# Kernel optimization log

Measured on AMD Instinct MI355X. Metric: run time of the kernel, lower is better.

Reference implementation:

```python
import jax, jax.numpy as jnp
import numpy as np

D = 100  # hidden dim: kernel has 3*D = 300 entries (concat(a, b, a*b))


def setup_inputs() -> dict:
    key = jax.random.key(0)
    k1, k2, k3 = jax.random.split(key, 3)
    context = jax.random.normal(k1, (16384, D), dtype=jnp.float32)
    question = jax.random.normal(k2, (4096, D), dtype=jnp.float32)
    kernel = jax.random.normal(k3, (3 * D,), dtype=jnp.float32)
    return {"context": context, "question": question, "kernel": kernel}


def reference(context, question, kernel):
    # kernel . concat(a, b, a*b) = a.w1 + b.w2 + (a*b).w3, computed without
    # materializing the [N, M, 3D] feature tensor.
    w1, w2, w3 = kernel[:D], kernel[D:2 * D], kernel[2 * D:]
    # S: [N, M] similarity matrix
    S = (context @ w1)[:, None] + (question @ w2)[None, :] \
        + (context * w3) @ question.T
    # C2Q: row-softmax over question positions, weighted sum of question
    A = jax.nn.softmax(S, axis=-1)            # [N, M]
    U_A = A @ question                          # [N, D]
    # Q2C: softmax over per-row maxes, weighted sum of context, tiled to rows
    b = jax.nn.softmax(jnp.max(S, axis=-1))    # [N]
    h = b @ context                             # [D]
    H_A = jnp.broadcast_to(h, context.shape)   # [N, D]
    # megamerge: [N, 4D]
    G = jnp.concatenate([context, U_A, context * U_A, context * H_A], axis=-1)
    return G
```

## Files before the change

### kernel.cpp

```cpp
#include <hip/hip_runtime.h>

typedef _Float16 f16x8 __attribute__((ext_vector_type(8)));
typedef float    f32x4 __attribute__((ext_vector_type(4)));
typedef float    f32x16 __attribute__((ext_vector_type(16)));
typedef unsigned int u32;

#define N_CTX 16384
#define N_Q   4096
#define DIM   100
#define THR   4.0f

union FragU { unsigned int u[4]; f16x8 v; };

#define MFMA32(a, b, c) __builtin_amdgcn_mfma_f32_32x32x16_f16((a), (b), (c), 0, 0, 0)
#define GLOAD_LDS(g, l) __builtin_amdgcn_global_load_lds( \
    (const __attribute__((address_space(1))) u32*)(const void*)(g), \
    (__attribute__((address_space(3))) u32*)(void*)(l), 16, 0, 0)

__global__ void prep_all(const float* __restrict__ q, const float* __restrict__ ctx,
                         const float* __restrict__ ker,
                         unsigned short* __restrict__ qbS, unsigned short* __restrict__ qTS,
                         unsigned short* __restrict__ cbH, float* __restrict__ a) {
    int b = blockIdx.x;
    int tid = threadIdx.x;
    if (b < 16) {
        int j = b * 256 + tid;
        const float* row = q + (size_t)j * DIM;
        float buf[100];
        float acc = 0.f;
        #pragma unroll
        for (int d4 = 0; d4 < 25; ++d4) {
            #pragma unroll
            for (int e = 0; e < 4; ++e) {
                float v = row[4 * d4 + e];
                buf[4 * d4 + e] = v;
                acc += v * ker[100 + 4 * d4 + e];
            }
        }
        char* img = (char*)qbS + (size_t)(j >> 5) * 8192 + (j & 31) * 16;
        #pragma unroll
        for (int o = 0; o < 16; ++o) {
            f16x8 h;
            #pragma unroll
            for (int e = 0; e < 8; ++e) {
                int d = 8 * o + e;
                float v = (d < DIM) ? buf[d] : (d == DIM ? acc : 0.f);
                h[e] = (_Float16)v;
            }
            *reinterpret_cast<f16x8*>(img + o * 512) = h;
        }
    } else if (b < 80) {
        int i = (b - 16) * 256 + tid;
        const float* row = ctx + (size_t)i * DIM;
        float acc = 0.f;
        #pragma unroll
        for (int d = 0; d < DIM; ++d) acc += row[d] * ker[d];
        a[i] = acc;
    } else if (b < 144) {
        int i = (b - 80) * 256 + tid;
        const float* row = ctx + (size_t)i * DIM;
        unsigned short* orow = cbH + (size_t)i * 128;
        #pragma unroll
        for (int c = 0; c < 16; ++c) {
            f16x8 h;
            #pragma unroll
            for (int e = 0; e < 8; ++e) {
                int d = 8 * c + e;
                float v = (d < DIM) ? row[d] * ker[200 + d] : (d == DIM ? 1.f : 0.f);
                h[e] = (_Float16)v;
            }
            *reinterpret_cast<f16x8*>(orow + 8 * c) = h;
        }
    } else {
        __shared__ _Float16 ldsT[100][64];
        int j0 = (b - 144) * 64;
        int r = tid >> 2, c = tid & 3;
        const float* row = q + (size_t)(j0 + r) * DIM + c * 25;
        #pragma unroll
        for (int k = 0; k < 25; ++k) ldsT[c * 25 + k][r] = (_Float16)row[k];
        __syncthreads();
        #pragma unroll
        for (int k = 0; k < 4; ++k) {
            int ci = tid + k * 256;
            int jb = ci >> 9;
            int rem = ci & 511;
            int dt = rem >> 7, rem2 = rem & 127;
            int o = rem2 >> 5, rr = rem2 & 31;
            int d = dt * 32 + rr;
            f16x8 v;
            #pragma unroll
            for (int e = 0; e < 8; ++e) {
                int jl = jb * 32 + 8 * o + e;
                v[e] = (d < DIM) ? ldsT[d][jl] : (d == DIM ? (_Float16)1.f : (_Float16)0.f);
            }
            char* dst = (char*)qTS + (size_t)((j0 >> 5) + jb) * 8192
                        + dt * 2048 + o * 512 + rr * 16;
            *reinterpret_cast<f16x8*>(dst) = v;
        }
    }
}

__global__ __launch_bounds__(256, 4) void attn_main(
    const unsigned short* __restrict__ qbS, const unsigned short* __restrict__ qTS,
    const unsigned short* __restrict__ cbH,
    _Float16* __restrict__ Ub, float* __restrict__ mb,
    float* __restrict__ lb, float* __restrict__ mtb)
{
    __shared__ __align__(16) char stageMem[2][16384];

    const int tid  = threadIdx.x;
    const int w    = tid >> 6;
    const int lane = tid & 63;
    const int hi   = lane >> 5;
    const int c31  = lane & 31;
    const int it   = blockIdx.x;
    const int js   = blockIdx.y;
    const int JS   = gridDim.y;
    const int R    = (N_Q / 32) / JS;
    const int iw0  = it * 128 + w * 32;

    f16x8 cbF[7];
    {
        const unsigned short* crow = cbH + (size_t)(iw0 + c31) * 128 + 8 * hi;
        #pragma unroll
        for (int kk = 0; kk < 7; ++kk)
            cbF[kk] = *reinterpret_cast<const f16x8*>(crow + kk * 16);
    }

    f32x16 U0 = {}, U1 = {}, U2 = {}, U3 = {};
    float m = -INFINITY, mtrue = -INFINITY;

    const int bb0 = js * R;
    const int seg = w * 2;
    const int l16 = lane * 16;

    auto stage_fn = [&](int buf, int bb) {
        const char* gq = (const char*)qbS + (size_t)bb * 8192;
        const char* gt = (const char*)qTS + (size_t)bb * 8192;
        char* lq = stageMem[buf];
        #pragma unroll
        for (int k = 0; k < 2; ++k)
            GLOAD_LDS(gq + (seg + k) * 1024 + l16, lq + (seg + k) * 1024);
        #pragma unroll
        for (int k = 0; k < 2; ++k)
            GLOAD_LDS(gt + (seg + k) * 1024 + l16, lq + 8192 + (seg + k) * 1024);
    };

    stage_fn(0, bb0);
    __syncthreads();
    int cur = 0;

    for (int r = 0; r < R; ++r) {
        if (r + 1 < R) stage_fn(cur ^ 1, bb0 + r + 1);

        const char* qbL = stageMem[cur];
        const char* qTL = stageMem[cur] + 8192;

        f32x16 sacc = {};
        __builtin_amdgcn_s_setprio(1);
        #pragma unroll
        for (int kk = 0; kk < 7; ++kk) {
            f16x8 aq = *reinterpret_cast<const f16x8*>(qbL + kk * 1024 + l16);
            sacc = MFMA32(aq, cbF[kk], sacc);
        }
        __builtin_amdgcn_s_setprio(0);

        float sc[16];
        #pragma unroll
        for (int q16 = 0; q16 < 16; ++q16) sc[q16] = sacc[q16];

        float t0 = fmaxf(sc[0], sc[1]),  t1 = fmaxf(sc[2], sc[3]);
        float t2 = fmaxf(sc[4], sc[5]),  t3 = fmaxf(sc[6], sc[7]);
        float t4 = fmaxf(sc[8], sc[9]),  t5 = fmaxf(sc[10], sc[11]);
        float t6 = fmaxf(sc[12], sc[13]), t7 = fmaxf(sc[14], sc[15]);
        t0 = fmaxf(t0, t1); t2 = fmaxf(t2, t3);
        t4 = fmaxf(t4, t5); t6 = fmaxf(t6, t7);
        float tm = fmaxf(fmaxf(t0, t2), fmaxf(t4, t6));
        mtrue = fmaxf(mtrue, tm);

        if (__any(tm > m + THR)) {
            float tmf = fmaxf(tm, __shfl_xor(tm, 32, 64));
            float mn = fmaxf(m, tmf);
            float scale = __expf(m - mn);
            U0 *= scale; U1 *= scale; U2 *= scale; U3 *= scale;
            m = mn;
        }

        #pragma unroll
        for (int q16 = 0; q16 < 16; ++q16) sc[q16] = __expf(sc[q16] - m);

        unsigned int pk[8], pr[8];
        #pragma unroll
        for (int h2 = 0; h2 < 8; ++h2) {
            auto p2 = __builtin_amdgcn_cvt_pkrtz(sc[2 * h2], sc[2 * h2 + 1]);
            pk[h2] = __builtin_bit_cast(unsigned int, p2);
            pr[h2] = (unsigned int)__shfl_xor((int)pk[h2], 32, 64);
        }
        FragU f0, f1;
        f0.u[0] = hi ? pr[2] : pk[0];
        f0.u[1] = hi ? pr[3] : pk[1];
        f0.u[2] = hi ? pk[2] : pr[0];
        f0.u[3] = hi ? pk[3] : pr[1];
        f1.u[0] = hi ? pr[6] : pk[4];
        f1.u[1] = hi ? pr[7] : pk[5];
        f1.u[2] = hi ? pk[6] : pr[4];
        f1.u[3] = hi ? pk[7] : pr[5];

        __builtin_amdgcn_s_setprio(1);
        {
            f16x8 a0 = *reinterpret_cast<const f16x8*>(qTL + l16);
            f16x8 a1 = *reinterpret_cast<const f16x8*>(qTL + 1024 + l16);
            U0 = MFMA32(a0, f0.v, U0);
            U0 = MFMA32(a1, f1.v, U0);
        }
        {
            f16x8 a0 = *reinterpret_cast<const f16x8*>(qTL + 2048 + l16);
            f16x8 a1 = *reinterpret_cast<const f16x8*>(qTL + 3072 + l16);
            U1 = MFMA32(a0, f0.v, U1);
            U1 = MFMA32(a1, f1.v, U1);
        }
        {
            f16x8 a0 = *reinterpret_cast<const f16x8*>(qTL + 4096 + l16);
            f16x8 a1 = *reinterpret_cast<const f16x8*>(qTL + 5120 + l16);
            U2 = MFMA32(a0, f0.v, U2);
            U2 = MFMA32(a1, f1.v, U2);
        }
        {
            f16x8 a0 = *reinterpret_cast<const f16x8*>(qTL + 6144 + l16);
            f16x8 a1 = *reinterpret_cast<const f16x8*>(qTL + 7168 + l16);
            U3 = MFMA32(a0, f0.v, U3);
            U3 = MFMA32(a1, f1.v, U3);
        }
        __builtin_amdgcn_s_setprio(0);

        __syncthreads();
        cur ^= 1;
    }

    mtrue = fmaxf(mtrue, __shfl_xor(mtrue, 32, 64));
    float ltmp = __shfl_xor(U3[0], 32, 64);
    float lfull = hi ? U3[0] : ltmp;

    int irow = iw0 + c31;
    if (hi == 0) {
        mb [(size_t)js * N_CTX + irow] = m;
        lb [(size_t)js * N_CTX + irow] = lfull;
        mtb[(size_t)js * N_CTX + irow] = mtrue;
    }
    _Float16* ub = Ub + (((size_t)js * 128 + it) * DIM) * 128 + w * 32 + c31;
    #pragma unroll
    for (int r = 0; r < 16; ++r) {
        int dl = (r & 3) + 8 * (r >> 2) + 4 * hi;
        ub[(size_t)dl * 128]        = (_Float16)U0[r];
        ub[(size_t)(32 + dl) * 128] = (_Float16)U1[r];
        ub[(size_t)(64 + dl) * 128] = (_Float16)U2[r];
        if (96 + dl < DIM) ub[(size_t)(96 + dl) * 128] = (_Float16)U3[r];
    }
}


template<int JS>
__global__ void kernel_mf(const float* __restrict__ a, const float* __restrict__ mtb,
                          float* __restrict__ mfull) {
    int i = blockIdx.x * 256 + threadIdx.x;
    float mt = -INFINITY;
    #pragma unroll
    for (int js = 0; js < JS; ++js) mt = fmaxf(mt, mtb[(size_t)js * N_CTX + i]);
    mfull[i] = a[i] + mt;
}

__global__ void kernel_h(const float* __restrict__ mfull, const float* __restrict__ ctx,
                         float* __restrict__ hp) {
    __shared__ float sm[256];
    __shared__ float smh[8][104];
    int t = threadIdx.x;
    float v = -INFINITY;
    for (int i = t; i < N_CTX; i += 256) v = fmaxf(v, mfull[i]);
    sm[t] = v; __syncthreads();
    for (int s = 128; s > 0; s >>= 1) { if (t < s) sm[t] = fmaxf(sm[t], sm[t + s]); __syncthreads(); }
    float M = sm[0];
    __syncthreads();
    float z = 0.f;
    for (int i = t; i < N_CTX; i += 256) z += __expf(mfull[i] - M);
    sm[t] = z; __syncthreads();
    for (int s = 128; s > 0; s >>= 1) { if (t < s) sm[t] += sm[t + s]; __syncthreads(); }
    float Z = sm[0];
    __syncthreads();

    int rr = t >> 5, d32 = t & 31;
    int i0 = blockIdx.x * 64;
    float a0 = 0.f, a1 = 0.f, a2 = 0.f, a3 = 0.f;
    for (int g = 0; g < 8; ++g) {
        int row = i0 + g * 8 + rr;
        float bw = __expf(mfull[row] - M);
        const float* cr = ctx + (size_t)row * DIM;
        a0 += bw * cr[d32];
        a1 += bw * cr[d32 + 32];
        a2 += bw * cr[d32 + 64];
        if (d32 < 4) a3 += bw * cr[d32 + 96];
    }
    smh[rr][d32]      = a0;
    smh[rr][d32 + 32] = a1;
    smh[rr][d32 + 64] = a2;
    if (d32 < 4) smh[rr][d32 + 96] = a3;
    __syncthreads();
    if (t < DIM) {
        float s = 0.f;
        #pragma unroll
        for (int g = 0; g < 8; ++g) s += smh[g][t];
        hp[blockIdx.x * 128 + t] = s / Z;
    }
}

__global__ void kernel_hred(const float* __restrict__ hp, float* __restrict__ h) {
    __shared__ float sm[4][128];
    int t = threadIdx.x;
    int d = t & 127, rep = t >> 7;
    float s = 0.f;
    if (d < DIM) for (int b = 0; b < 64; ++b) s += hp[(rep * 64 + b) * 128 + d];
    sm[rep][d] = s;
    __syncthreads();
    if (rep == 0 && d < DIM) h[d] = sm[0][d] + sm[1][d] + sm[2][d] + sm[3][d];
}

template<int JS>
__global__ __launch_bounds__(256, 4) void combine(
    const _Float16* __restrict__ Ub, const float* __restrict__ mb,
    const float* __restrict__ lb, const float* __restrict__ h,
    const float* __restrict__ ctx, float* __restrict__ G)
{
    __shared__ float ctxL[32][100];
    __shared__ float uaL[32][100];
    __shared__ float hL[100];

    const int b   = blockIdx.x;
    const int tid = threadIdx.x;

    for (int idx = tid; idx < 32 * DIM; idx += 256) {
        int r = idx / DIM, d = idx - r * DIM;
        ctxL[r][d] = ctx[(size_t)(b * 32 + r) * DIM + d];
    }
    if (tid < DIM) hL[tid] = h[tid];
    __syncthreads();

    {
        int i32 = tid & 31, seg = tid >> 5;
        int row = b * 32 + i32;
        int iblk = row >> 7, il = row & 127;
        float mw[JS];
        float M = -INFINITY;
        #pragma unroll
        for (int js = 0; js < JS; ++js) {
            mw[js] = mb[(size_t)js * N_CTX + row];
            M = fmaxf(M, mw[js]);
        }
        float ew[JS];
        float L = 0.f;
        #pragma unroll
        for (int js = 0; js < JS; ++js) {
            ew[js] = __expf(mw[js] - M);
            L += lb[(size_t)js * N_CTX + row] * ew[js];
        }
        float invL = 1.f / L;
        for (int d = seg; d < DIM; d += 8) {
            float u = 0.f;
            #pragma unroll
            for (int js = 0; js < JS; ++js)
                u += (float)Ub[(((size_t)js * 128 + iblk) * DIM + d) * 128 + il] * ew[js];
            uaL[i32][d] = u * invL;
        }
    }
    __syncthreads();

    float* gOut = G + (size_t)b * 32 * 400;
    for (int idx = tid; idx < 32 * 400; idx += 256) {
        int r = idx / 400, c = idx - r * 400;
        int sel = c / 100, d = c - sel * 100;
        float cv = ctxL[r][d];
        float val;
        if (sel == 0)      val = cv;
        else if (sel == 1) val = uaL[r][d];
        else if (sel == 2) val = uaL[r][d] * cv;
        else               val = cv * hL[d];
        gOut[idx] = val;
    }
}

extern "C" void kernel_launch(void* const* d_in, const int* in_sizes, int n_in,
                              void* d_out, int out_size, void* d_ws, size_t ws_size,
                              hipStream_t stream) {
    const float* ctx = (const float*)d_in[0];
    const float* q   = (const float*)d_in[1];
    const float* ker = (const float*)d_in[2];
    float* G = (float*)d_out;

    char* ws = (char*)d_ws;
    unsigned short* qbS   = (unsigned short*)(ws);
    unsigned short* qTS   = (unsigned short*)(ws + 1048576);
    unsigned short* cbH   = (unsigned short*)(ws + 2097152);
    float*          a     = (float*)(ws + 6291456);
    float*          mfull = (float*)(ws + 6356992);
    float*          hp    = (float*)(ws + 6422528);
    float*          h     = (float*)(ws + 6553600);
    const size_t fixed = 6554112;

    int JS = 8;
    if (fixed + 8ull * 3473408ull > ws_size) JS = 4;
    if (fixed + 4ull * 3473408ull > ws_size) JS = 2;

    _Float16* Ub  = (_Float16*)(ws + fixed);
    size_t ubB    = (size_t)JS * 3276800ull;
    float*    mb  = (float*)(ws + fixed + ubB);
    float*    lb  = (float*)(ws + fixed + ubB + (size_t)JS * 65536ull);
    float*    mtb = (float*)(ws + fixed + ubB + (size_t)JS * 131072ull);

    prep_all<<<dim3(208), dim3(256), 0, stream>>>(q, ctx, ker, qbS, qTS, cbH, a);
    attn_main<<<dim3(128, JS), dim3(256), 0, stream>>>(qbS, qTS, cbH, Ub, mb, lb, mtb);

    if (JS == 8) {
        kernel_mf<8><<<dim3(64), dim3(256), 0, stream>>>(a, mtb, mfull);
        kernel_h<<<dim3(256), dim3(256), 0, stream>>>(mfull, ctx, hp);
        kernel_hred<<<dim3(1), dim3(512), 0, stream>>>(hp, h);
        combine<8><<<dim3(512), dim3(256), 0, stream>>>(Ub, mb, lb, h, ctx, G);
    } else if (JS == 4) {
        kernel_mf<4><<<dim3(64), dim3(256), 0, stream>>>(a, mtb, mfull);
        kernel_h<<<dim3(256), dim3(256), 0, stream>>>(mfull, ctx, hp);
        kernel_hred<<<dim3(1), dim3(512), 0, stream>>>(hp, h);
        combine<4><<<dim3(512), dim3(256), 0, stream>>>(Ub, mb, lb, h, ctx, G);
    } else {
        kernel_mf<2><<<dim3(64), dim3(256), 0, stream>>>(a, mtb, mfull);
        kernel_h<<<dim3(256), dim3(256), 0, stream>>>(mfull, ctx, hp);
        kernel_hred<<<dim3(1), dim3(512), 0, stream>>>(hp, h);
        combine<2><<<dim3(512), dim3(256), 0, stream>>>(Ub, mb, lb, h, ctx, G);
    }
}
```

Measured before the change: 111.0 us.

## Merge ctx prep blocks, split MFMA accumulator chain, fold h-reduction into combine

Merges the two context-row prep branches so each context row is read once, computing both the w1 dot product and the fp16 w3-scaled row from a register buffer, which cuts prep_all from 208 to 144 blocks. The score MFMA chain is split across two independent accumulators, which are summed afterwards, to shorten the dependent MFMA latency chain. The single-block kernel_hred launch is removed, and every combine block now sums the 256 partial h vectors itself. That saves a launch and a serialization point, but every combine block repeats the 256-element reduction per dimension.

```diff
diff --git a/kernel.cpp b/kernel.cpp
--- a/kernel.cpp
+++ b/kernel.cpp
@@ -52,13 +52,18 @@
     } else if (b < 80) {
         int i = (b - 16) * 256 + tid;
         const float* row = ctx + (size_t)i * DIM;
+        float buf[100];
         float acc = 0.f;
         #pragma unroll
-        for (int d = 0; d < DIM; ++d) acc += row[d] * ker[d];
+        for (int d4 = 0; d4 < 25; ++d4) {
+            #pragma unroll
+            for (int e = 0; e < 4; ++e) {
+                float v = row[4 * d4 + e];
+                buf[4 * d4 + e] = v;
+                acc += v * ker[4 * d4 + e];
+            }
+        }
         a[i] = acc;
-    } else if (b < 144) {
-        int i = (b - 80) * 256 + tid;
-        const float* row = ctx + (size_t)i * DIM;
         unsigned short* orow = cbH + (size_t)i * 128;
         #pragma unroll
         for (int c = 0; c < 16; ++c) {
@@ -66,14 +71,14 @@
             #pragma unroll
             for (int e = 0; e < 8; ++e) {
                 int d = 8 * c + e;
-                float v = (d < DIM) ? row[d] * ker[200 + d] : (d == DIM ? 1.f : 0.f);
+                float v = (d < DIM) ? buf[d] * ker[200 + d] : (d == DIM ? 1.f : 0.f);
                 h[e] = (_Float16)v;
             }
             *reinterpret_cast<f16x8*>(orow + 8 * c) = h;
         }
     } else {
         __shared__ _Float16 ldsT[100][64];
-        int j0 = (b - 144) * 64;
+        int j0 = (b - 80) * 64;
         int r = tid >> 2, c = tid & 3;
         const float* row = q + (size_t)(j0 + r) * DIM + c * 25;
         #pragma unroll
@@ -156,18 +161,29 @@
         const char* qbL = stageMem[cur];
         const char* qTL = stageMem[cur] + 8192;
 
-        f32x16 sacc = {};
+        f32x16 sa = {}, sb = {};
         __builtin_amdgcn_s_setprio(1);
-        #pragma unroll
-        for (int kk = 0; kk < 7; ++kk) {
-            f16x8 aq = *reinterpret_cast<const f16x8*>(qbL + kk * 1024 + l16);
-            sacc = MFMA32(aq, cbF[kk], sacc);
+        {
+            f16x8 aq0 = *reinterpret_cast<const f16x8*>(qbL + 0 * 1024 + l16);
+            f16x8 aq1 = *reinterpret_cast<const f16x8*>(qbL + 1 * 1024 + l16);
+            f16x8 aq2 = *reinterpret_cast<const f16x8*>(qbL + 2 * 1024 + l16);
+            f16x8 aq3 = *reinterpret_cast<const f16x8*>(qbL + 3 * 1024 + l16);
+            f16x8 aq4 = *reinterpret_cast<const f16x8*>(qbL + 4 * 1024 + l16);
+            f16x8 aq5 = *reinterpret_cast<const f16x8*>(qbL + 5 * 1024 + l16);
+            f16x8 aq6 = *reinterpret_cast<const f16x8*>(qbL + 6 * 1024 + l16);
+            sa = MFMA32(aq0, cbF[0], sa);
+            sb = MFMA32(aq1, cbF[1], sb);
+            sa = MFMA32(aq2, cbF[2], sa);
+            sb = MFMA32(aq3, cbF[3], sb);
+            sa = MFMA32(aq4, cbF[4], sa);
+            sb = MFMA32(aq5, cbF[5], sb);
+            sa = MFMA32(aq6, cbF[6], sa);
         }
         __builtin_amdgcn_s_setprio(0);
 
         float sc[16];
         #pragma unroll
-        for (int q16 = 0; q16 < 16; ++q16) sc[q16] = sacc[q16];
+        for (int q16 = 0; q16 < 16; ++q16) sc[q16] = sa[q16] + sb[q16];
 
         float t0 = fmaxf(sc[0], sc[1]),  t1 = fmaxf(sc[2], sc[3]);
         float t2 = fmaxf(sc[4], sc[5]),  t3 = fmaxf(sc[6], sc[7]);
@@ -312,21 +328,10 @@
     }
 }
 
-__global__ void kernel_hred(const float* __restrict__ hp, float* __restrict__ h) {
-    __shared__ float sm[4][128];
-    int t = threadIdx.x;
-    int d = t & 127, rep = t >> 7;
-    float s = 0.f;
-    if (d < DIM) for (int b = 0; b < 64; ++b) s += hp[(rep * 64 + b) * 128 + d];
-    sm[rep][d] = s;
-    __syncthreads();
-    if (rep == 0 && d < DIM) h[d] = sm[0][d] + sm[1][d] + sm[2][d] + sm[3][d];
-}
-
 template<int JS>
 __global__ __launch_bounds__(256, 4) void combine(
     const _Float16* __restrict__ Ub, const float* __restrict__ mb,
-    const float* __restrict__ lb, const float* __restrict__ h,
+    const float* __restrict__ lb, const float* __restrict__ hp,
     const float* __restrict__ ctx, float* __restrict__ G)
 {
     __shared__ float ctxL[32][100];
@@ -340,7 +345,11 @@
         int r = idx / DIM, d = idx - r * DIM;
         ctxL[r][d] = ctx[(size_t)(b * 32 + r) * DIM + d];
     }
-    if (tid < DIM) hL[tid] = h[tid];
+    if (tid < DIM) {
+        float s = 0.f;
+        for (int bb = 0; bb < 256; ++bb) s += hp[bb * 128 + tid];
+        hL[tid] = s;
+    }
     __syncthreads();
 
     {
@@ -401,7 +410,6 @@
     float*          a     = (float*)(ws + 6291456);
     float*          mfull = (float*)(ws + 6356992);
     float*          hp    = (float*)(ws + 6422528);
-    float*          h     = (float*)(ws + 6553600);
     const size_t fixed = 6554112;
 
     int JS = 8;
@@ -414,23 +422,20 @@
     float*    lb  = (float*)(ws + fixed + ubB + (size_t)JS * 65536ull);
     float*    mtb = (float*)(ws + fixed + ubB + (size_t)JS * 131072ull);
 
-    prep_all<<<dim3(208), dim3(256), 0, stream>>>(q, ctx, ker, qbS, qTS, cbH, a);
+    prep_all<<<dim3(144), dim3(256), 0, stream>>>(q, ctx, ker, qbS, qTS, cbH, a);
     attn_main<<<dim3(128, JS), dim3(256), 0, stream>>>(qbS, qTS, cbH, Ub, mb, lb, mtb);
 
     if (JS == 8) {
         kernel_mf<8><<<dim3(64), dim3(256), 0, stream>>>(a, mtb, mfull);
         kernel_h<<<dim3(256), dim3(256), 0, stream>>>(mfull, ctx, hp);
-        kernel_hred<<<dim3(1), dim3(512), 0, stream>>>(hp, h);
-        combine<8><<<dim3(512), dim3(256), 0, stream>>>(Ub, mb, lb, h, ctx, G);
+        combine<8><<<dim3(512), dim3(256), 0, stream>>>(Ub, mb, lb, hp, ctx, G);
     } else if (JS == 4) {
         kernel_mf<4><<<dim3(64), dim3(256), 0, stream>>>(a, mtb, mfull);
         kernel_h<<<dim3(256), dim3(256), 0, stream>>>(mfull, ctx, hp);
-        kernel_hred<<<dim3(1), dim3(512), 0, stream>>>(hp, h);
-        combine<4><<<dim3(512), dim3(256), 0, stream>>>(Ub, mb, lb, h, ctx, G);
+        combine<4><<<dim3(512), dim3(256), 0, stream>>>(Ub, mb, lb, hp, ctx, G);
     } else {
         kernel_mf<2><<<dim3(64), dim3(256), 0, stream>>>(a, mtb, mfull);
         kernel_h<<<dim3(256), dim3(256), 0, stream>>>(mfull, ctx, hp);
-        kernel_hred<<<dim3(1), dim3(512), 0, stream>>>(hp, h);
-        combine<2><<<dim3(512), dim3(256), 0, stream>>>(Ub, mb, lb, h, ctx, G);
-    }
-}
+        combine<2><<<dim3(512), dim3(256), 0, stream>>>(Ub, mb, lb, hp, ctx, G);
+    }
+}
```

New measurement: 120.6 us. +8.6%, slower.
